# Optimization experiments

Hardware: AMD Instinct MI355X
Metric: run time of the kernel (lower is better)

Reference implementation:

```python
import math
import jax, jax.numpy as jnp
import numpy as np

B, L, D, H = 4, 512, 256, 8
DH = D // H
BUCKETS = 11  # rel_pos_buckets; padding_idx = BUCKETS


def setup_inputs() -> dict:
    key = jax.random.key(0)
    ks = jax.random.split(key, 12)
    s = 0.02
    rel_table = jax.random.normal(ks[10], (BUCKETS + 1, D), dtype=jnp.float32) * s
    rel_table = rel_table.at[BUCKETS].set(0.0)  # padding_idx row is zero
    return {
        "inputs": jax.random.normal(ks[0], (B, L, D), dtype=jnp.float32),
        "mask": jax.random.randint(ks[1], (B, L, L), 0, 2) > 0,
        "distances": jax.random.randint(ks[2], (B, L, L), 0, BUCKETS + 1),
        "Wq": jax.random.normal(ks[3], (D, D), dtype=jnp.float32) * s,
        "bq": jnp.zeros((D,), jnp.float32),
        "Wk": jax.random.normal(ks[4], (D, D), dtype=jnp.float32) * s,
        "bk": jnp.zeros((D,), jnp.float32),
        "Wv": jax.random.normal(ks[5], (D, D), dtype=jnp.float32) * s,
        "bv": jnp.zeros((D,), jnp.float32),
        "Wo": jax.random.normal(ks[6], (D, D), dtype=jnp.float32) * s,
        "bo": jnp.zeros((D,), jnp.float32),
        "rel_table": rel_table,
        "u": jax.random.normal(ks[7], (D,), dtype=jnp.float32) * s,
        "v": jax.random.normal(ks[8], (D,), dtype=jnp.float32) * s,
    }


def reference(inputs, mask, distances, Wq, bq, Wk, bk, Wv, bv, Wo, bo, rel_table, u, v):
    def shape(x):  # (B, L, D) -> (B, H, L, DH)
        return x.reshape(B, L, H, DH).transpose(0, 2, 1, 3)

    q = shape(inputs @ Wq + bq) / math.sqrt(DH)
    k = shape(inputs @ Wk + bk)
    val = shape(inputs @ Wv + bv)

    # content term: (q + u) k^T
    a_c = jnp.einsum("bhqd,bhkd->bhqk", q + u.reshape(1, H, 1, DH), k)

    # relative-position term: embedding gather (padding row already zero, mask anyway)
    valid = (distances != BUCKETS)[..., None].astype(rel_table.dtype)
    rel = (rel_table[distances] * valid).reshape(B, L, L, H, DH)  # (B, Lq, Lk, H, DH)
    b_d = jnp.einsum("bhqd,bqkhd->bhqk", q + v.reshape(1, H, 1, DH), rel)

    scores = jnp.where(mask[:, None, :, :], jnp.float32(-1e18), a_c + b_d)
    attn = jax.nn.softmax(scores, axis=-1)  # (B, H, Lq, Lk)

    ctx = jnp.einsum("bhqk,bhkd->bhqd", attn, val)
    ctx = ctx.transpose(0, 2, 1, 3).reshape(B, L, D)
    output = ctx @ Wo + bo
    return output, attn
```

## Files before the change

### kernel.cpp

```cpp
#include <hip/hip_runtime.h>
#include <math.h>

#define BB 4
#define LL 512
#define DD 256
#define HH 8
#define DHH 32
#define NB 12

__global__ __launch_bounds__(256) void qkv_kernel(const float* __restrict__ x,
    const float* __restrict__ Wq, const float* __restrict__ bq,
    const float* __restrict__ Wk, const float* __restrict__ bk,
    const float* __restrict__ Wv, const float* __restrict__ bv,
    const float* __restrict__ uvec, const float* __restrict__ vvec,
    float* __restrict__ Qu, float* __restrict__ Qv,
    float* __restrict__ KT, float* __restrict__ V) {
    __shared__ float xs[8][DD];
    const int mat = blockIdx.x >> 8;
    const int r0 = (blockIdx.x & 255) * 8;
    const int t = threadIdx.x;
    const int cg = t & 63, rg = t >> 6;
    const int c0 = cg * 4;
    {
        const float4* xg = (const float4*)(x + r0 * DD);
        float4* xsv = (float4*)&xs[0][0];
        xsv[t] = xg[t];
        xsv[t + 256] = xg[t + 256];
    }
    __syncthreads();
    const float* W    = (mat == 0) ? Wq : (mat == 1) ? Wk : Wv;
    const float* bias = (mat == 0) ? bq : (mat == 1) ? bk : bv;
    float acc[2][4];
#pragma unroll
    for (int r = 0; r < 2; ++r)
#pragma unroll
        for (int c = 0; c < 4; ++c) acc[r][c] = bias[c0 + c];
    for (int i0 = 0; i0 < DD; i0 += 4) {
        float4 wv4[4], xv4[2];
#pragma unroll
        for (int j = 0; j < 4; ++j) wv4[j] = *(const float4*)&W[(i0 + j) * DD + c0];
#pragma unroll
        for (int r = 0; r < 2; ++r) xv4[r] = *(const float4*)&xs[rg * 2 + r][i0];
        const float* wf = (const float*)wv4;
        const float* xf = (const float*)xv4;
#pragma unroll
        for (int r = 0; r < 2; ++r)
#pragma unroll
            for (int j = 0; j < 4; ++j)
#pragma unroll
                for (int c = 0; c < 4; ++c)
                    acc[r][c] = fmaf(xf[r * 4 + j], wf[j * 4 + c], acc[r][c]);
    }
    if (mat == 0) {
        const float s = 0.17677669529663687f;
        const float4 u4 = *(const float4*)&uvec[c0];
        const float4 v4 = *(const float4*)&vvec[c0];
#pragma unroll
        for (int r = 0; r < 2; ++r) {
            const int row = r0 + rg * 2 + r;
            float4 q = make_float4(acc[r][0] * s, acc[r][1] * s, acc[r][2] * s, acc[r][3] * s);
            *(float4*)&Qu[row * DD + c0] = make_float4(q.x + u4.x, q.y + u4.y, q.z + u4.z, q.w + u4.w);
            *(float4*)&Qv[row * DD + c0] = make_float4(q.x + v4.x, q.y + v4.y, q.z + v4.z, q.w + v4.w);
        }
    } else if (mat == 1) {
        const int b = r0 >> 9;
        const int kb = (r0 & 511) + rg * 2;
#pragma unroll
        for (int c = 0; c < 4; ++c) {
            const int col = c0 + c;
            const int h = col >> 5, dd = col & 31;
            float* p = KT + ((long)((b * HH + h) * DHH + dd)) * LL + kb;
            p[0] = acc[0][c];
            p[1] = acc[1][c];
        }
    } else {
#pragma unroll
        for (int r = 0; r < 2; ++r)
            *(float4*)&V[(r0 + rg * 2 + r) * DD + c0] =
                make_float4(acc[r][0], acc[r][1], acc[r][2], acc[r][3]);
    }
}

__global__ __launch_bounds__(512, 6) void scores_ctx_kernel(const float* __restrict__ Qu,
    const float* __restrict__ Qv, const float* __restrict__ KT,
    const float* __restrict__ rel_table, const int* __restrict__ mask,
    const int* __restrict__ dist, const float* __restrict__ V,
    float* __restrict__ attn, float* __restrict__ ctx) {
    __shared__ float Qs[16][DHH];
    __shared__ float Qv8[16][DHH];
    __shared__ float rels[NB][DHH + 1];
    __shared__ float Ps[16][NB];
    __shared__ float Ss[16][4][132];
    __shared__ float4 Cp[512];
    const int blk = blockIdx.x;
    const int h = blk & 7;
    const int rest = blk >> 3;
    const int qt = rest & 31;
    const int b = rest >> 5;
    const int q0 = qt * 16;
    const int t = threadIdx.x;
    const int w = t >> 6, l = t & 63;

    {
        const int r = t >> 5, c = t & 31;
        Qs[r][c]  = Qu[(b * LL + q0 + r) * DD + h * DHH + c];
        Qv8[r][c] = Qv[(b * LL + q0 + r) * DD + h * DHH + c];
    }
    if (t < NB * DHH) {
        rels[t >> 5][t & 31] = rel_table[(t >> 5) * DD + h * DHH + (t & 31)];
    }
    __syncthreads();
    if (t < 16 * NB) {
        const int bk = t >> 4, r = t & 15;
        float a = 0.f;
#pragma unroll
        for (int d = 0; d < DHH; ++d) a = fmaf(Qv8[r][d], rels[bk][d], a);
        Ps[r][bk] = a;
    }
    __syncthreads();

    const int r0 = 2 * w;
    const long kbase = (long)(b * HH + h) * DHH * LL;
    float e0[2][4], e1[2][4];
    float sum0 = 0.f, sum1 = 0.f;
#pragma unroll
    for (int s = 0; s < 2; ++s) {
        const int k0 = 4 * l + 256 * s;
        const int4 dx0 = *(const int4*)&dist[(b * LL + q0 + r0) * LL + k0];
        const int4 dx1 = *(const int4*)&dist[(b * LL + q0 + r0 + 1) * LL + k0];
        const int4 mx0 = *(const int4*)&mask[(b * LL + q0 + r0) * LL + k0];
        const int4 mx1 = *(const int4*)&mask[(b * LL + q0 + r0 + 1) * LL + k0];
        float s0[4], s1[4];
        s0[0] = Ps[r0][dx0.x]; s0[1] = Ps[r0][dx0.y]; s0[2] = Ps[r0][dx0.z]; s0[3] = Ps[r0][dx0.w];
        s1[0] = Ps[r0 + 1][dx1.x]; s1[1] = Ps[r0 + 1][dx1.y]; s1[2] = Ps[r0 + 1][dx1.z]; s1[3] = Ps[r0 + 1][dx1.w];
#pragma unroll
        for (int d4 = 0; d4 < DHH; d4 += 4) {
            const float4 q0v = *(const float4*)&Qs[r0][d4];
            const float4 q1v = *(const float4*)&Qs[r0 + 1][d4];
            float4 kv[4];
#pragma unroll
            for (int j = 0; j < 4; ++j)
                kv[j] = *(const float4*)&KT[kbase + (long)(d4 + j) * LL + k0];
            const float* qf0 = (const float*)&q0v;
            const float* qf1 = (const float*)&q1v;
#pragma unroll
            for (int j = 0; j < 4; ++j) {
                s0[0] = fmaf(qf0[j], kv[j].x, s0[0]);
                s0[1] = fmaf(qf0[j], kv[j].y, s0[1]);
                s0[2] = fmaf(qf0[j], kv[j].z, s0[2]);
                s0[3] = fmaf(qf0[j], kv[j].w, s0[3]);
                s1[0] = fmaf(qf1[j], kv[j].x, s1[0]);
                s1[1] = fmaf(qf1[j], kv[j].y, s1[1]);
                s1[2] = fmaf(qf1[j], kv[j].z, s1[2]);
                s1[3] = fmaf(qf1[j], kv[j].w, s1[3]);
            }
        }
        e0[s][0] = mx0.x ? 0.f : __expf(s0[0]);
        e0[s][1] = mx0.y ? 0.f : __expf(s0[1]);
        e0[s][2] = mx0.z ? 0.f : __expf(s0[2]);
        e0[s][3] = mx0.w ? 0.f : __expf(s0[3]);
        e1[s][0] = mx1.x ? 0.f : __expf(s1[0]);
        e1[s][1] = mx1.y ? 0.f : __expf(s1[1]);
        e1[s][2] = mx1.z ? 0.f : __expf(s1[2]);
        e1[s][3] = mx1.w ? 0.f : __expf(s1[3]);
        sum0 += (e0[s][0] + e0[s][1]) + (e0[s][2] + e0[s][3]);
        sum1 += (e1[s][0] + e1[s][1]) + (e1[s][2] + e1[s][3]);
    }
    for (int off = 32; off > 0; off >>= 1) {
        sum0 += __shfl_xor(sum0, off);
        sum1 += __shfl_xor(sum1, off);
    }
    const float i0 = 1.0f / sum0, i1 = 1.0f / sum1;
    float* a0 = attn + ((long)(b * HH + h) * LL + q0 + r0) * LL;
    float* a1 = a0 + LL;
#pragma unroll
    for (int s = 0; s < 2; ++s) {
        const int k0 = 4 * l + 256 * s;
        const int ch = k0 >> 7, off = k0 & 127;
        const float4 o0 = make_float4(e0[s][0] * i0, e0[s][1] * i0, e0[s][2] * i0, e0[s][3] * i0);
        const float4 o1 = make_float4(e1[s][0] * i1, e1[s][1] * i1, e1[s][2] * i1, e1[s][3] * i1);
        *(float4*)&a0[k0] = o0;
        *(float4*)&a1[k0] = o1;
        *(float4*)&Ss[r0][ch][off] = o0;
        *(float4*)&Ss[r0 + 1][ch][off] = o1;
    }
    __syncthreads();

    const int qB = t >> 5;
    const int ks = (t >> 3) & 3;
    const int dg = t & 7;
    const float* vb = V + ((long)(b * LL + ks * 128)) * DD + h * DHH + dg * 4;
    float4 acc = make_float4(0.f, 0.f, 0.f, 0.f);
    float4 vA[4], vB[4];
    float4 aA, aB;
#pragma unroll
    for (int j = 0; j < 4; ++j) vA[j] = *(const float4*)&vb[j * DD];
    aA = *(const float4*)&Ss[qB][ks][0];
    for (int kk = 0; kk < 128; kk += 8) {
#pragma unroll
        for (int j = 0; j < 4; ++j) vB[j] = *(const float4*)&vb[(kk + 4 + j) * DD];
        aB = *(const float4*)&Ss[qB][ks][kk + 4];
        acc.x = fmaf(aA.x, vA[0].x, fmaf(aA.y, vA[1].x, fmaf(aA.z, vA[2].x, fmaf(aA.w, vA[3].x, acc.x))));
        acc.y = fmaf(aA.x, vA[0].y, fmaf(aA.y, vA[1].y, fmaf(aA.z, vA[2].y, fmaf(aA.w, vA[3].y, acc.y))));
        acc.z = fmaf(aA.x, vA[0].z, fmaf(aA.y, vA[1].z, fmaf(aA.z, vA[2].z, fmaf(aA.w, vA[3].z, acc.z))));
        acc.w = fmaf(aA.x, vA[0].w, fmaf(aA.y, vA[1].w, fmaf(aA.z, vA[2].w, fmaf(aA.w, vA[3].w, acc.w))));
        if (kk + 8 < 128) {
#pragma unroll
            for (int j = 0; j < 4; ++j) vA[j] = *(const float4*)&vb[(kk + 8 + j) * DD];
            aA = *(const float4*)&Ss[qB][ks][kk + 8];
        }
        acc.x = fmaf(aB.x, vB[0].x, fmaf(aB.y, vB[1].x, fmaf(aB.z, vB[2].x, fmaf(aB.w, vB[3].x, acc.x))));
        acc.y = fmaf(aB.x, vB[0].y, fmaf(aB.y, vB[1].y, fmaf(aB.z, vB[2].y, fmaf(aB.w, vB[3].y, acc.y))));
        acc.z = fmaf(aB.x, vB[0].z, fmaf(aB.y, vB[1].z, fmaf(aB.z, vB[2].z, fmaf(aB.w, vB[3].z, acc.z))));
        acc.w = fmaf(aB.x, vB[0].w, fmaf(aB.y, vB[1].w, fmaf(aB.z, vB[2].w, fmaf(aB.w, vB[3].w, acc.w))));
    }
    Cp[t] = acc;
    __syncthreads();
    if (ks == 0) {
        const float4 c0 = Cp[t];
        const float4 c1 = Cp[t + 8];
        const float4 c2 = Cp[t + 16];
        const float4 c3 = Cp[t + 24];
        const float4 r = make_float4((c0.x + c1.x) + (c2.x + c3.x),
                                     (c0.y + c1.y) + (c2.y + c3.y),
                                     (c0.z + c1.z) + (c2.z + c3.z),
                                     (c0.w + c1.w) + (c2.w + c3.w));
        *(float4*)&ctx[(b * LL + q0 + qB) * DD + h * DHH + dg * 4] = r;
    }
}

__global__ __launch_bounds__(256) void outproj_kernel(const float* __restrict__ ctx,
    const float* __restrict__ Wo, const float* __restrict__ bo,
    float* __restrict__ out) {
    __shared__ float xs[4][DD];
    const int r0 = blockIdx.x * 4;
    const int t = threadIdx.x;
    const int rg = t >> 6;
    const int c0 = (t & 63) * 4;
    ((float4*)&xs[0][0])[t] = ((const float4*)(ctx + r0 * DD))[t];
    __syncthreads();
    float4 acc = *(const float4*)&bo[c0];
    for (int i0 = 0; i0 < DD; i0 += 8) {
        float4 wv[8];
#pragma unroll
        for (int j = 0; j < 8; ++j) wv[j] = *(const float4*)&Wo[(i0 + j) * DD + c0];
        const float4 x0 = *(const float4*)&xs[rg][i0];
        const float4 x1 = *(const float4*)&xs[rg][i0 + 4];
        const float* xf0 = (const float*)&x0;
        const float* xf1 = (const float*)&x1;
#pragma unroll
        for (int j = 0; j < 4; ++j) {
            acc.x = fmaf(xf0[j], wv[j].x, acc.x);
            acc.y = fmaf(xf0[j], wv[j].y, acc.y);
            acc.z = fmaf(xf0[j], wv[j].z, acc.z);
            acc.w = fmaf(xf0[j], wv[j].w, acc.w);
        }
#pragma unroll
        for (int j = 0; j < 4; ++j) {
            acc.x = fmaf(xf1[j], wv[j + 4].x, acc.x);
            acc.y = fmaf(xf1[j], wv[j + 4].y, acc.y);
            acc.z = fmaf(xf1[j], wv[j + 4].z, acc.z);
            acc.w = fmaf(xf1[j], wv[j + 4].w, acc.w);
        }
    }
    *(float4*)&out[(r0 + rg) * DD + c0] = acc;
}

extern "C" void kernel_launch(void* const* d_in, const int* in_sizes, int n_in,
                              void* d_out, int out_size, void* d_ws, size_t ws_size,
                              hipStream_t stream) {
    const float* x    = (const float*)d_in[0];
    const int* mk     = (const int*)d_in[1];
    const int* dist   = (const int*)d_in[2];
    const float* Wq = (const float*)d_in[3];
    const float* bq = (const float*)d_in[4];
    const float* Wk = (const float*)d_in[5];
    const float* bk = (const float*)d_in[6];
    const float* Wv = (const float*)d_in[7];
    const float* bv = (const float*)d_in[8];
    const float* Wo = (const float*)d_in[9];
    const float* bo = (const float*)d_in[10];
    const float* rel_table = (const float*)d_in[11];
    const float* uvec = (const float*)d_in[12];
    const float* vvec = (const float*)d_in[13];

    float* out  = (float*)d_out;
    float* attn = out + BB * LL * DD;

    float* Qu = (float*)d_ws;
    float* Qv = Qu + BB * LL * DD;
    float* KT = Qv + BB * LL * DD;
    float* V  = KT + BB * LL * DD;
    float* C  = V + BB * LL * DD;

    qkv_kernel<<<3 * 256, 256, 0, stream>>>(x, Wq, bq, Wk, bk, Wv, bv, uvec, vvec,
                                            Qu, Qv, KT, V);
    scores_ctx_kernel<<<BB * (LL / 16) * HH, 512, 0, stream>>>(Qu, Qv, KT, rel_table,
                                                               mk, dist, V, attn, C);
    outproj_kernel<<<BB * LL / 4, 256, 0, stream>>>(C, Wo, bo, out);
}
```

Measured before the change: 186.9 us.

## Stage V tiles in shared memory for attention-times-V and drop partial reduction

The attn·V stage is restructured. Each 128-key chunk of V for the head is loaded once per block into a transposed shared-memory tile. Each thread then computes one full ctx element over all keys, which removes the per-thread strided global V reads and the cross-thread partial-sum reduction buffer. The QK^T loop is also widened to load 8 K rows at a time, and the launch-bounds occupancy hint drops from 6 to 4. The cost is extra barriers per chunk, and float4 reads from a row stride of 133 floats that may be misaligned or bank-conflicted.

```diff
diff --git a/kernel.cpp b/kernel.cpp
--- a/kernel.cpp
+++ b/kernel.cpp
@@ -81,7 +81,7 @@
     }
 }
 
-__global__ __launch_bounds__(512, 6) void scores_ctx_kernel(const float* __restrict__ Qu,
+__global__ __launch_bounds__(512, 4) void scores_ctx_kernel(const float* __restrict__ Qu,
     const float* __restrict__ Qv, const float* __restrict__ KT,
     const float* __restrict__ rel_table, const int* __restrict__ mask,
     const int* __restrict__ dist, const float* __restrict__ V,
@@ -91,7 +91,7 @@
     __shared__ float rels[NB][DHH + 1];
     __shared__ float Ps[16][NB];
     __shared__ float Ss[16][4][132];
-    __shared__ float4 Cp[512];
+    __shared__ float Vs[DHH][133];
     const int blk = blockIdx.x;
     const int h = blk & 7;
     const int rest = blk >> 3;
@@ -134,25 +134,40 @@
         s0[0] = Ps[r0][dx0.x]; s0[1] = Ps[r0][dx0.y]; s0[2] = Ps[r0][dx0.z]; s0[3] = Ps[r0][dx0.w];
         s1[0] = Ps[r0 + 1][dx1.x]; s1[1] = Ps[r0 + 1][dx1.y]; s1[2] = Ps[r0 + 1][dx1.z]; s1[3] = Ps[r0 + 1][dx1.w];
 #pragma unroll
-        for (int d4 = 0; d4 < DHH; d4 += 4) {
-            const float4 q0v = *(const float4*)&Qs[r0][d4];
-            const float4 q1v = *(const float4*)&Qs[r0 + 1][d4];
-            float4 kv[4];
-#pragma unroll
-            for (int j = 0; j < 4; ++j)
-                kv[j] = *(const float4*)&KT[kbase + (long)(d4 + j) * LL + k0];
-            const float* qf0 = (const float*)&q0v;
-            const float* qf1 = (const float*)&q1v;
+        for (int d8 = 0; d8 < DHH; d8 += 8) {
+            float4 kv[8];
+#pragma unroll
+            for (int j = 0; j < 8; ++j)
+                kv[j] = *(const float4*)&KT[kbase + (long)(d8 + j) * LL + k0];
+            const float4 q0a = *(const float4*)&Qs[r0][d8];
+            const float4 q0b = *(const float4*)&Qs[r0][d8 + 4];
+            const float4 q1a = *(const float4*)&Qs[r0 + 1][d8];
+            const float4 q1b = *(const float4*)&Qs[r0 + 1][d8 + 4];
+            const float* qa0 = (const float*)&q0a;
+            const float* qb0 = (const float*)&q0b;
+            const float* qa1 = (const float*)&q1a;
+            const float* qb1 = (const float*)&q1b;
 #pragma unroll
             for (int j = 0; j < 4; ++j) {
-                s0[0] = fmaf(qf0[j], kv[j].x, s0[0]);
-                s0[1] = fmaf(qf0[j], kv[j].y, s0[1]);
-                s0[2] = fmaf(qf0[j], kv[j].z, s0[2]);
-                s0[3] = fmaf(qf0[j], kv[j].w, s0[3]);
-                s1[0] = fmaf(qf1[j], kv[j].x, s1[0]);
-                s1[1] = fmaf(qf1[j], kv[j].y, s1[1]);
-                s1[2] = fmaf(qf1[j], kv[j].z, s1[2]);
-                s1[3] = fmaf(qf1[j], kv[j].w, s1[3]);
+                s0[0] = fmaf(qa0[j], kv[j].x, s0[0]);
+                s0[1] = fmaf(qa0[j], kv[j].y, s0[1]);
+                s0[2] = fmaf(qa0[j], kv[j].z, s0[2]);
+                s0[3] = fmaf(qa0[j], kv[j].w, s0[3]);
+                s1[0] = fmaf(qa1[j], kv[j].x, s1[0]);
+                s1[1] = fmaf(qa1[j], kv[j].y, s1[1]);
+                s1[2] = fmaf(qa1[j], kv[j].z, s1[2]);
+                s1[3] = fmaf(qa1[j], kv[j].w, s1[3]);
+            }
+#pragma unroll
+            for (int j = 0; j < 4; ++j) {
+                s0[0] = fmaf(qb0[j], kv[j + 4].x, s0[0]);
+                s0[1] = fmaf(qb0[j], kv[j + 4].y, s0[1]);
+                s0[2] = fmaf(qb0[j], kv[j + 4].z, s0[2]);
+                s0[3] = fmaf(qb0[j], kv[j + 4].w, s0[3]);
+                s1[0] = fmaf(qb1[j], kv[j + 4].x, s1[0]);
+                s1[1] = fmaf(qb1[j], kv[j + 4].y, s1[1]);
+                s1[2] = fmaf(qb1[j], kv[j + 4].z, s1[2]);
+                s1[3] = fmaf(qb1[j], kv[j + 4].w, s1[3]);
             }
         }
         e0[s][0] = mx0.x ? 0.f : __expf(s0[0]);
@@ -184,49 +199,32 @@
         *(float4*)&Ss[r0][ch][off] = o0;
         *(float4*)&Ss[r0 + 1][ch][off] = o1;
     }
-    __syncthreads();
 
     const int qB = t >> 5;
-    const int ks = (t >> 3) & 3;
-    const int dg = t & 7;
-    const float* vb = V + ((long)(b * LL + ks * 128)) * DD + h * DHH + dg * 4;
-    float4 acc = make_float4(0.f, 0.f, 0.f, 0.f);
-    float4 vA[4], vB[4];
-    float4 aA, aB;
-#pragma unroll
-    for (int j = 0; j < 4; ++j) vA[j] = *(const float4*)&vb[j * DD];
-    aA = *(const float4*)&Ss[qB][ks][0];
-    for (int kk = 0; kk < 128; kk += 8) {
-#pragma unroll
-        for (int j = 0; j < 4; ++j) vB[j] = *(const float4*)&vb[(kk + 4 + j) * DD];
-        aB = *(const float4*)&Ss[qB][ks][kk + 4];
-        acc.x = fmaf(aA.x, vA[0].x, fmaf(aA.y, vA[1].x, fmaf(aA.z, vA[2].x, fmaf(aA.w, vA[3].x, acc.x))));
-        acc.y = fmaf(aA.x, vA[0].y, fmaf(aA.y, vA[1].y, fmaf(aA.z, vA[2].y, fmaf(aA.w, vA[3].y, acc.y))));
-        acc.z = fmaf(aA.x, vA[0].z, fmaf(aA.y, vA[1].z, fmaf(aA.z, vA[2].z, fmaf(aA.w, vA[3].z, acc.z))));
-        acc.w = fmaf(aA.x, vA[0].w, fmaf(aA.y, vA[1].w, fmaf(aA.z, vA[2].w, fmaf(aA.w, vA[3].w, acc.w))));
-        if (kk + 8 < 128) {
-#pragma unroll
-            for (int j = 0; j < 4; ++j) vA[j] = *(const float4*)&vb[(kk + 8 + j) * DD];
-            aA = *(const float4*)&Ss[qB][ks][kk + 8];
-        }
-        acc.x = fmaf(aB.x, vB[0].x, fmaf(aB.y, vB[1].x, fmaf(aB.z, vB[2].x, fmaf(aB.w, vB[3].x, acc.x))));
-        acc.y = fmaf(aB.x, vB[0].y, fmaf(aB.y, vB[1].y, fmaf(aB.z, vB[2].y, fmaf(aB.w, vB[3].y, acc.y))));
-        acc.z = fmaf(aB.x, vB[0].z, fmaf(aB.y, vB[1].z, fmaf(aB.z, vB[2].z, fmaf(aB.w, vB[3].z, acc.z))));
-        acc.w = fmaf(aB.x, vB[0].w, fmaf(aB.y, vB[1].w, fmaf(aB.z, vB[2].w, fmaf(aB.w, vB[3].w, acc.w))));
-    }
-    Cp[t] = acc;
-    __syncthreads();
-    if (ks == 0) {
-        const float4 c0 = Cp[t];
-        const float4 c1 = Cp[t + 8];
-        const float4 c2 = Cp[t + 16];
-        const float4 c3 = Cp[t + 24];
-        const float4 r = make_float4((c0.x + c1.x) + (c2.x + c3.x),
-                                     (c0.y + c1.y) + (c2.y + c3.y),
-                                     (c0.z + c1.z) + (c2.z + c3.z),
-                                     (c0.w + c1.w) + (c2.w + c3.w));
-        *(float4*)&ctx[(b * LL + q0 + qB) * DD + h * DHH + dg * 4] = r;
-    }
+    const int dB = t & 31;
+    const int kkS = t >> 2;
+    const int dqS = (t & 3) * 8;
+    float acc = 0.f;
+    for (int c = 0; c < 4; ++c) {
+        __syncthreads();
+        {
+            const float* vg = V + ((long)(b * LL + c * 128 + kkS)) * DD + h * DHH + dqS;
+            const float4 va = *(const float4*)&vg[0];
+            const float4 vb4 = *(const float4*)&vg[4];
+            Vs[dqS + 0][kkS] = va.x;  Vs[dqS + 1][kkS] = va.y;
+            Vs[dqS + 2][kkS] = va.z;  Vs[dqS + 3][kkS] = va.w;
+            Vs[dqS + 4][kkS] = vb4.x; Vs[dqS + 5][kkS] = vb4.y;
+            Vs[dqS + 6][kkS] = vb4.z; Vs[dqS + 7][kkS] = vb4.w;
+        }
+        __syncthreads();
+#pragma unroll
+        for (int j = 0; j < 32; ++j) {
+            const float4 sv = *(const float4*)&Ss[qB][c][4 * j];
+            const float4 vv = *(const float4*)&Vs[dB][4 * j];
+            acc = fmaf(sv.x, vv.x, fmaf(sv.y, vv.y, fmaf(sv.z, vv.z, fmaf(sv.w, vv.w, acc))));
+        }
+    }
+    ctx[(b * LL + q0 + qB) * DD + h * DHH + dB] = acc;
 }
 
 __global__ __launch_bounds__(256) void outproj_kernel(const float* __restrict__ ctx,
```

Result: faster. 179.8 us (-3.8%).
